# Optimization experiments

Hardware: AMD Instinct MI355X
Metric: run time of the kernel (lower is better)

Reference implementation:

```python
import jax, jax.numpy as jnp
import numpy as np

EP = 0.1
BETA = 10.0
ALPHA = 2.0
LMDA = 1.0
GROUP = 5  # 1 anchor + 4 positives per identity group


def setup_inputs() -> dict:
    key = jax.random.key(0)
    k1, k2 = jax.random.split(key)
    inputs = jax.random.normal(k1, (20480, 512), dtype=jnp.float32)
    targets = jax.random.randint(k2, (20480,), 0, 751, dtype=jnp.int64)
    return {"inputs": inputs, "targets": targets}


def reference(inputs, targets):
    B, D = inputs.shape
    N = B // GROUP  # number of anchor groups
    # f.data in torch detaches the anchor side; gradient flows only via inputs.T
    f = jax.lax.stop_gradient(inputs[0::GROUP])          # (N, D)
    sim = jnp.matmul(f, inputs.T)                         # (N, B)
    sim_r = sim.reshape(N, N, GROUP)                      # sim_r[k, j, r] = sim[k, 5j+r]

    idx = jnp.arange(N)
    # positives: sim[k, 5k+1 : 5k+5]  -> (N, 4)
    pos = sim_r[idx, idx, 1:GROUP]
    # own-group mask (anchor's entire group of 5 is excluded from negatives)
    own = (jnp.eye(N, dtype=bool))[:, :, None]            # (N, N, 1) broadcast over r

    neg_inf = jnp.finfo(sim.dtype).min
    neg_max = jnp.where(own, neg_inf, sim_r).max(axis=(1, 2))   # (N,)
    pos_min = pos.min(axis=1)                                    # (N,)

    # positive branch: keep pos_sim < neg_max + ep
    p_mask = pos < (neg_max[:, None] + EP)                       # (N, 4)
    loss_p = jnp.log1p(jnp.sum(jnp.where(p_mask, jnp.exp(-ALPHA * (pos - LMDA)), 0.0), axis=1)) / ALPHA

    # negative branch: keep neg_sim > pos_min - ep, over all other groups
    n_mask = (sim_r > (pos_min[:, None, None] - EP)) & (~own)    # (N, N, 5)
    loss_n = jnp.log1p(jnp.sum(jnp.where(n_mask, jnp.exp(BETA * (sim_r - LMDA)), 0.0), axis=(1, 2))) / BETA

    loss = jnp.sum(loss_p + loss_n) / N                          # matches loss / f.shape[0]
    p_num = jnp.sum(p_mask).astype(jnp.float32)
    n_num = jnp.sum(n_mask).astype(jnp.float32)
    p_ratio = p_num / (4.0 * N)
    n_ratio = n_num / (float(B - GROUP) * N)
    return loss, p_ratio, n_ratio
```

## Files before the change

### kernel.cpp

```cpp
#include <hip/hip_runtime.h>
#include <hip/hip_bf16.h>
#include <math.h>

#define NB    4096
#define BB    20480
#define DD    512
#define EPc    0.1f
#define BETAc  10.0f
#define ALPHAc 2.0f
#define LMDAc  1.0f
#define SHIFT  1400.0

typedef __attribute__((ext_vector_type(8))) short bf16x8;
typedef __attribute__((ext_vector_type(4))) float f32x4;
typedef unsigned int u32;

#define GLOAD16(gp, lp) \
    __builtin_amdgcn_global_load_lds((const __attribute__((address_space(1))) u32*)(gp), \
                                     (__attribute__((address_space(3))) u32*)(lp), 16, 0, 0)

__device__ __forceinline__ unsigned fenc(float x) {
    unsigned b = __float_as_uint(x);
    return (b & 0x80000000u) ? ~b : (b | 0x80000000u);
}
__device__ __forceinline__ float fdec(unsigned k) {
    unsigned b = (k & 0x80000000u) ? (k ^ 0x80000000u) : ~k;
    return __uint_as_float(b);
}

__device__ __forceinline__ void split2(float a, float b, u32* h, u32* l) {
    __hip_bfloat16 ha = __float2bfloat16(a);
    __hip_bfloat16 hb = __float2bfloat16(b);
    unsigned short ba, bb;
    __builtin_memcpy(&ba, &ha, 2); __builtin_memcpy(&bb, &hb, 2);
    float fa = __uint_as_float((u32)ba << 16);
    float fb = __uint_as_float((u32)bb << 16);
    __hip_bfloat16 la = __float2bfloat16(a - fa);
    __hip_bfloat16 lb = __float2bfloat16(b - fb);
    unsigned short ca, cb;
    __builtin_memcpy(&ca, &la, 2); __builtin_memcpy(&cb, &lb, 2);
    *h = (u32)ba | ((u32)bb << 16);
    *l = (u32)ca | ((u32)cb << 16);
}

__device__ __forceinline__ uint4 cvt8_sel(const float* __restrict__ src, bool lo_part) {
    float4 x0 = *(const float4*)(src);
    float4 x1 = *(const float4*)(src + 4);
    float xs[8] = {x0.x, x0.y, x0.z, x0.w, x1.x, x1.y, x1.z, x1.w};
    u32 w[4];
    #pragma unroll
    for (int p = 0; p < 4; ++p) {
        u32 h, l;
        split2(xs[2*p], xs[2*p+1], &h, &l);
        w[p] = lo_part ? l : h;
    }
    return make_uint4(w[0], w[1], w[2], w[3]);
}

__global__ __launch_bounds__(256) void packA_kernel(const float* __restrict__ inp,
        u32* __restrict__ apk)
{
    const u32 slot = blockIdx.x * 256 + threadIdx.x;
    const u32 lane = slot & 63;
    const u32 rest = slot >> 6;
    const u32 kc   = rest % 48;
    const u32 ablk = rest / 48;
    const int  i    = ablk * 16 + (lane & 15);
    const int  k0   = (kc % 16) * 32 + (lane >> 4) * 8;
    const bool lo_p = ((kc / 16) == 1);
    uint4 v = cvt8_sel(inp + (size_t)(5 * i) * DD + k0, lo_p);
    *(uint4*)(apk + (size_t)slot * 4) = v;
}

__global__ __launch_bounds__(256) void packB_kernel(const float* __restrict__ inp,
        u32* __restrict__ bpk)
{
    const u32 slot = blockIdx.x * 256 + threadIdx.x;
    const u32 lane = slot & 63;
    const u32 rest = slot >> 6;
    const u32 kc   = rest % 48;
    const u32 cblk = rest / 48;
    const int  r    = cblk * 16 + (lane & 15);
    const int  k0   = (kc % 16) * 32 + (lane >> 4) * 8;
    const bool lo_p = ((kc / 16) == 2);
    uint4 v = cvt8_sel(inp + (size_t)r * DD + k0, lo_p);
    *(uint4*)(bpk + (size_t)slot * 4) = v;
}

__global__ __launch_bounds__(256) void split_kernel(const float* __restrict__ inp,
        u32* __restrict__ hi, u32* __restrict__ lo)
{
    const size_t e = ((size_t)blockIdx.x * 256 + threadIdx.x) * 8;
    float4 x0 = *(const float4*)(inp + e);
    float4 x1 = *(const float4*)(inp + e + 4);
    u32 h[4], l[4];
    split2(x0.x, x0.y, &h[0], &l[0]);
    split2(x0.z, x0.w, &h[1], &l[1]);
    split2(x1.x, x1.y, &h[2], &l[2]);
    split2(x1.z, x1.w, &h[3], &l[3]);
    *(uint4*)(hi + e / 2) = make_uint4(h[0], h[1], h[2], h[3]);
    *(uint4*)(lo + e / 2) = make_uint4(l[0], l[1], l[2], l[3]);
}

__global__ __launch_bounds__(256) void pos_kernel(const float* __restrict__ inp,
        float* __restrict__ pos, float* __restrict__ posmin)
{
    const int wid  = threadIdx.x >> 6;
    const int lane = threadIdx.x & 63;
    const int i = blockIdx.x * 4 + wid;
    const float* f = inp + (size_t)(5 * i) * DD + lane * 8;
    float4 fa = *(const float4*)(f);
    float4 fb = *(const float4*)(f + 4);
    float pmin = INFINITY;
    #pragma unroll
    for (int g = 1; g < 5; ++g) {
        const float* x = inp + (size_t)(5 * i + g) * DD + lane * 8;
        float4 xa = *(const float4*)(x);
        float4 xb = *(const float4*)(x + 4);
        float s = fa.x*xa.x + fa.y*xa.y + fa.z*xa.z + fa.w*xa.w
                + fb.x*xb.x + fb.y*xb.y + fb.z*xb.z + fb.w*xb.w;
        #pragma unroll
        for (int m = 1; m < 64; m <<= 1) s += __shfl_xor(s, m, 64);
        if (lane == 0) pos[i * 4 + (g - 1)] = s;
        pmin = fminf(pmin, s);
    }
    if (lane == 0) posmin[i] = pmin;
}

__device__ __forceinline__ void row_epilogue(int i, int c0, int wc, int l15,
        float s0, float s1, float s2, float s3,
        const float* __restrict__ posmin, unsigned* __restrict__ negkey,
        double* __restrict__ msum, unsigned* __restrict__ cntn)
{
    const float th = posmin[i] - EPc;
    float vmax = -INFINITY;
    float lM   = -INFINITY;
    float lS   = 0.f;
    int   vcnt = 0;
    float sv[4] = {s0, s1, s2, s3};
    float args[4]; bool msk[4];
    #pragma unroll
    for (int fc = 0; fc < 4; ++fc) {
        const int c = c0 + wc + fc * 16 + l15;
        const float s = sv[fc];
        const bool nonown = ((c / 5) != i);
        msk[fc]  = nonown && (s > th);
        args[fc] = BETAc * (s - LMDAc);
        if (nonown)  vmax = fmaxf(vmax, s);
        if (msk[fc]) { vcnt += 1; lM = fmaxf(lM, args[fc]); }
    }
    #pragma unroll
    for (int fc = 0; fc < 4; ++fc)
        if (msk[fc]) lS += __expf(args[fc] - lM);
    #pragma unroll
    for (int m = 1; m < 16; m <<= 1) {
        vmax  = fmaxf(vmax, __shfl_xor(vmax, m, 64));
        vcnt += __shfl_xor(vcnt, m, 64);
        float oM = __shfl_xor(lM, m, 64);
        float oS = __shfl_xor(lS, m, 64);
        if (oS != 0.f) {
            if (lS == 0.f)      { lM = oM; lS = oS; }
            else if (lM >= oM)  { lS += oS * __expf(oM - lM); }
            else                { lS = oS + lS * __expf(lM - oM); lM = oM; }
        }
    }
    if (l15 == 0) {
        atomicMax(&negkey[i], fenc(vmax));
        atomicAdd(&cntn[i], (unsigned)vcnt);
        if (lS > 0.f) {
            double e = (double)lM - SHIFT;
            if (e > 690.0) e = 690.0;
            double Dv = exp(e) * (double)lS;
            if (!(Dv < 1e300)) Dv = 1e300;
            atomicAdd(&msum[i], Dv);
        }
    }
}

__global__ __launch_bounds__(256, 3) void sim_mfma10(const u32* __restrict__ apk,
        const u32* __restrict__ bpk, const float* __restrict__ posmin,
        unsigned* __restrict__ negkey, double* __restrict__ msum,
        unsigned* __restrict__ cntn)
{
    const int t    = threadIdx.x;
    const int lane = t & 63;
    const int w    = t >> 6;
    const int l15  = lane & 15;
    const int l4   = lane >> 4;

    const int bid   = blockIdx.x;
    const int xcd   = bid & 7;
    const int r_    = bid >> 3;
    const int chunk = r_ >> 4;
    const int pos   = r_ & 15;
    const int gc    = xcd * 40 + chunk;
    const int bi    = (gc & 7) * 4 + (pos & 3);
    const int bj    = (gc >> 3) * 4 + (pos >> 2);
    const int i0    = bi * 128;
    const int c0    = bj * 128;
    const int wr    = (w >> 1) * 64;
    const int wc    = (w & 1) * 64;

    const u32* pa[4];
    const u32* pb[4];
    #pragma unroll
    for (int f = 0; f < 4; ++f) {
        const int ablk = bi * 8 + (w >> 1) * 4 + f;
        const int cblk = bj * 8 + (w & 1) * 4 + f;
        pa[f] = apk + ((size_t)ablk * 48 * 64 + lane) * 4;
        pb[f] = bpk + ((size_t)cblk * 48 * 64 + lane) * 4;
    }

    f32x4 acc[4][4];
    #pragma unroll
    for (int a = 0; a < 4; ++a)
        #pragma unroll
        for (int b = 0; b < 4; ++b) acc[a][b] = (f32x4)0.f;

#define LOADF(AV, BV, KC) do {                                           \
    _Pragma("unroll")                                                    \
    for (int f_ = 0; f_ < 4; ++f_) (AV)[f_] = *(const bf16x8*)(pa[f_] + (KC) * 256); \
    _Pragma("unroll")                                                    \
    for (int f_ = 0; f_ < 4; ++f_) (BV)[f_] = *(const bf16x8*)(pb[f_] + (KC) * 256); \
} while (0)

#define MMB(AV, BV) do {                                                 \
    __builtin_amdgcn_s_setprio(1);                                       \
    _Pragma("unroll")                                                    \
    for (int fr_ = 0; fr_ < 4; ++fr_)                                    \
        _Pragma("unroll")                                                \
        for (int fc_ = 0; fc_ < 4; ++fc_)                                \
            acc[fr_][fc_] = __builtin_amdgcn_mfma_f32_16x16x32_bf16(     \
                (AV)[fr_], (BV)[fc_], acc[fr_][fc_], 0, 0, 0);           \
    __builtin_amdgcn_s_setprio(0);                                       \
} while (0)

    bf16x8 a0[4], b0[4], a1[4], b1[4];
    LOADF(a0, b0, 0);
    #pragma unroll 1
    for (int kc = 0; kc < 48; kc += 2) {
        LOADF(a1, b1, kc + 1);
        MMB(a0, b0);
        if (kc + 2 < 48) LOADF(a0, b0, kc + 2);
        MMB(a1, b1);
    }
#undef LOADF
#undef MMB

    #pragma unroll
    for (int fr = 0; fr < 4; ++fr) {
        #pragma unroll
        for (int reg = 0; reg < 4; ++reg) {
            const int i = i0 + wr + fr * 16 + l4 * 4 + reg;
            row_epilogue(i, c0, wc, l15,
                         acc[fr][0][reg], acc[fr][1][reg],
                         acc[fr][2][reg], acc[fr][3][reg],
                         posmin, negkey, msum, cntn);
        }
    }
}

__global__ __launch_bounds__(256) void sim_mfma7(const u32* __restrict__ hi,
        const u32* __restrict__ lo, const float* __restrict__ posmin,
        unsigned* __restrict__ negkey, double* __restrict__ msum,
        unsigned* __restrict__ cntn)
{
    __shared__ u32 As0[2048], Bs0[2048];
    __shared__ u32 As1[2048], Bs1[2048];

    const int t    = threadIdx.x;
    const int bj   = blockIdx.x % (BB / 128);
    const int bi   = blockIdx.x / (BB / 128);
    const int i0   = bi * 128;
    const int c0   = bj * 128;
    const int lane = t & 63;
    const int w    = t >> 6;
    const int wr   = (w >> 1) * 64;
    const int wc   = (w & 1) * 64;
    const int l15  = lane & 15;
    const int l4   = lane >> 4;

    const int srow = w * 32 + (lane >> 2);
    const int sc   = (lane & 3) ^ ((srow >> 1) & 3);
    const size_t rbA0 = (size_t)(5 * (i0 + srow))      * 1024 + sc * 16;
    const size_t rbA1 = (size_t)(5 * (i0 + srow + 16)) * 1024 + sc * 16;
    const size_t rbB0 = (size_t)(c0 + srow)      * 1024 + sc * 16;
    const size_t rbB1 = (size_t)(c0 + srow + 16) * 1024 + sc * 16;
    const int dL0 = (w * 32) * 16;
    const int dL1 = (w * 32 + 16) * 16;

#define STAGE(AS, BS, s) do {                                            \
    const int p_ = (s) >> 4;                                             \
    const size_t kk_ = (size_t)((s) & 15) * 64;                          \
    const char* bA_ = (const char*)(p_ == 1 ? lo : hi);                  \
    const char* bB_ = (const char*)(p_ == 2 ? lo : hi);                  \
    GLOAD16(bA_ + rbA0 + kk_, (AS) + dL0);                               \
    GLOAD16(bA_ + rbA1 + kk_, (AS) + dL1);                               \
    GLOAD16(bB_ + rbB0 + kk_, (BS) + dL0);                               \
    GLOAD16(bB_ + rbB1 + kk_, (BS) + dL1);                               \
} while (0)

    f32x4 acc[4][4];
    #pragma unroll
    for (int a = 0; a < 4; ++a)
        #pragma unroll
        for (int b = 0; b < 4; ++b) acc[a][b] = (f32x4)0.f;

    int aoff[4], boff[4];
    #pragma unroll
    for (int f = 0; f < 4; ++f) {
        const int row = wr + f * 16 + l15;
        const int col = wc + f * 16 + l15;
        aoff[f] = row * 64 + ((l4 ^ ((row >> 1) & 3)) * 16);
        boff[f] = col * 64 + ((l4 ^ ((col >> 1) & 3)) * 16);
    }

#define COMPUTE(AS, BS) do {                                             \
    bf16x8 bv[4];                                                        \
    _Pragma("unroll")                                                    \
    for (int fc = 0; fc < 4; ++fc)                                       \
        bv[fc] = *(const bf16x8*)((const char*)(BS) + boff[fc]);         \
    _Pragma("unroll")                                                    \
    for (int fr = 0; fr < 4; ++fr) {                                     \
        bf16x8 av = *(const bf16x8*)((const char*)(AS) + aoff[fr]);      \
        _Pragma("unroll")                                                \
        for (int fc = 0; fc < 4; ++fc)                                   \
            acc[fr][fc] = __builtin_amdgcn_mfma_f32_16x16x32_bf16(av, bv[fc], acc[fr][fc], 0, 0, 0); \
    }                                                                    \
} while (0)

#define VMCNT4  asm volatile("s_waitcnt vmcnt(4)" ::: "memory")
#define VMCNT0  asm volatile("s_waitcnt vmcnt(0)" ::: "memory")
#define MFENCE  asm volatile("" ::: "memory")
#define BARRIER __builtin_amdgcn_s_barrier()

    STAGE(As0, Bs0, 0);
    STAGE(As1, Bs1, 1);
    for (int it = 0; it < 23; ++it) {
        VMCNT4; BARRIER; MFENCE;
        COMPUTE(As0, Bs0);
        BARRIER; MFENCE;
        STAGE(As0, Bs0, 2 * it + 2);
        VMCNT4; BARRIER; MFENCE;
        COMPUTE(As1, Bs1);
        BARRIER; MFENCE;
        STAGE(As1, Bs1, 2 * it + 3);
    }
    VMCNT4; BARRIER; MFENCE;
    COMPUTE(As0, Bs0);
    VMCNT0; BARRIER; MFENCE;
    COMPUTE(As1, Bs1);

#undef STAGE
#undef COMPUTE
#undef VMCNT4
#undef VMCNT0
#undef MFENCE
#undef BARRIER

    #pragma unroll
    for (int fr = 0; fr < 4; ++fr) {
        #pragma unroll
        for (int reg = 0; reg < 4; ++reg) {
            const int i = i0 + wr + fr * 16 + l4 * 4 + reg;
            row_epilogue(i, c0, wc, l15,
                         acc[fr][0][reg], acc[fr][1][reg],
                         acc[fr][2][reg], acc[fr][3][reg],
                         posmin, negkey, msum, cntn);
        }
    }
}

__device__ __forceinline__ void cvt8(const float* __restrict__ src,
                                     uint4* __restrict__ dhi, uint4* __restrict__ dlo)
{
    float4 x0 = *(const float4*)(src);
    float4 x1 = *(const float4*)(src + 4);
    float xs[8] = {x0.x, x0.y, x0.z, x0.w, x1.x, x1.y, x1.z, x1.w};
    u32 h[4], l[4];
    #pragma unroll
    for (int p = 0; p < 4; ++p) split2(xs[2*p], xs[2*p+1], &h[p], &l[p]);
    *dhi = make_uint4(h[0], h[1], h[2], h[3]);
    *dlo = make_uint4(l[0], l[1], l[2], l[3]);
}

__global__ __launch_bounds__(256) void sim_mfma(const float* __restrict__ inp,
        const float* __restrict__ posmin, unsigned* __restrict__ negkey,
        double* __restrict__ msum, unsigned* __restrict__ cntn)
{
    __shared__ uint4 AsHi[128][4];
    __shared__ uint4 AsLo[128][4];
    __shared__ uint4 BsHi[128][4];
    __shared__ uint4 BsLo[128][4];

    const int t    = threadIdx.x;
    const int bj   = blockIdx.x % (BB / 128);
    const int bi   = blockIdx.x / (BB / 128);
    const int i0   = bi * 128;
    const int c0   = bj * 128;
    const int lane = t & 63;
    const int w    = t >> 6;
    const int wr   = (w >> 1) * 64;
    const int wc   = (w & 1) * 64;
    const int l15  = lane & 15;
    const int l4   = lane >> 4;

    f32x4 acc[4][4];
    #pragma unroll
    for (int a = 0; a < 4; ++a)
        #pragma unroll
        for (int b = 0; b < 4; ++b) acc[a][b] = (f32x4)0.f;

    const int r0  = t >> 2;
    const int ch0 = t & 3;

    for (int kb = 0; kb < DD; kb += 32) {
        __syncthreads();
        #pragma unroll
        for (int half = 0; half < 2; ++half) {
            const int row = r0 + half * 64;
            const int cs  = ch0 ^ ((row >> 2) & 3);
            cvt8(inp + (size_t)(5 * (i0 + row)) * DD + kb + ch0 * 8,
                 &AsHi[row][cs], &AsLo[row][cs]);
            cvt8(inp + (size_t)(c0 + row) * DD + kb + ch0 * 8,
                 &BsHi[row][cs], &BsLo[row][cs]);
        }
        __syncthreads();

        bf16x8 bh[4], bl[4];
        #pragma unroll
        for (int fc = 0; fc < 4; ++fc) {
            const int col = wc + fc * 16 + l15;
            const int cs  = l4 ^ ((col >> 2) & 3);
            bh[fc] = *(const bf16x8*)&BsHi[col][cs];
            bl[fc] = *(const bf16x8*)&BsLo[col][cs];
        }
        #pragma unroll
        for (int fr = 0; fr < 4; ++fr) {
            const int row = wr + fr * 16 + l15;
            const int cs  = l4 ^ ((row >> 2) & 3);
            bf16x8 ah = *(const bf16x8*)&AsHi[row][cs];
            bf16x8 al = *(const bf16x8*)&AsLo[row][cs];
            #pragma unroll
            for (int fc = 0; fc < 4; ++fc) {
                acc[fr][fc] = __builtin_amdgcn_mfma_f32_16x16x32_bf16(ah, bh[fc], acc[fr][fc], 0, 0, 0);
                acc[fr][fc] = __builtin_amdgcn_mfma_f32_16x16x32_bf16(ah, bl[fc], acc[fr][fc], 0, 0, 0);
                acc[fr][fc] = __builtin_amdgcn_mfma_f32_16x16x32_bf16(al, bh[fc], acc[fr][fc], 0, 0, 0);
            }
        }
    }

    #pragma unroll
    for (int fr = 0; fr < 4; ++fr) {
        #pragma unroll
        for (int reg = 0; reg < 4; ++reg) {
            const int i = i0 + wr + fr * 16 + l4 * 4 + reg;
            row_epilogue(i, c0, wc, l15,
                         acc[fr][0][reg], acc[fr][1][reg],
                         acc[fr][2][reg], acc[fr][3][reg],
                         posmin, negkey, msum, cntn);
        }
    }
}

__global__ __launch_bounds__(1024) void fin_kernel(const float* __restrict__ pos,
        const unsigned* __restrict__ negkey, const double* __restrict__ msum,
        const unsigned* __restrict__ cntn, float* __restrict__ out)
{
    const int t = threadIdx.x;
    double lossAcc = 0.0;
    int pAcc = 0, nAcc = 0;
    for (int r = t; r < NB; r += 1024) {
        const float negmax = fdec(negkey[r]);
        const float thr = negmax + EPc;
        float Mp = -INFINITY; int pc = 0;
        float pa[4]; bool pm[4];
        #pragma unroll
        for (int g = 0; g < 4; ++g) {
            const float p = pos[r * 4 + g];
            pa[g] = -ALPHAc * (p - LMDAc);
            pm[g] = (p < thr);
            if (pm[g]) { pc += 1; Mp = fmaxf(Mp, pa[g]); }
        }
        double lp = 0.0;
        if (pc > 0) {
            float sp = 0.f;
            #pragma unroll
            for (int g = 0; g < 4; ++g)
                if (pm[g]) sp += __expf(pa[g] - Mp);
            double a = (double)Mp + log((double)sp);
            lp = (a > 30.0 ? a : log1p(exp(a))) / (double)ALPHAc;
        }
        double ln = 0.0;
        double Dsum = msum[r];
        if (Dsum > 0.0) {
            double a = SHIFT + log(Dsum);
            ln = (a > 30.0 ? a : log1p(exp(a))) / (double)BETAc;
        }
        double contrib = lp + ln;
        if (!(contrib < 1e30)) contrib = 1e30;
        lossAcc += contrib;
        pAcc += pc;
        nAcc += (int)cntn[r];
    }
    __shared__ double sl[1024];
    __shared__ int    sp_[1024];
    __shared__ int    sn_[1024];
    sl[t] = lossAcc; sp_[t] = pAcc; sn_[t] = nAcc;
    __syncthreads();
    for (int s = 512; s > 0; s >>= 1) {
        if (t < s) { sl[t] += sl[t + s]; sp_[t] += sp_[t + s]; sn_[t] += sn_[t + s]; }
        __syncthreads();
    }
    if (t == 0) {
        double loss = sl[0] / 4096.0;
        if (!(loss < 1e30)) loss = 1e30;
        out[0] = (float)loss;
        out[1] = (float)sp_[0] / 16384.0f;
        out[2] = (float)sn_[0] / 83865600.0f;
    }
}

extern "C" void kernel_launch(void* const* d_in, const int* in_sizes, int n_in,
                              void* d_out, int out_size, void* d_ws, size_t ws_size,
                              hipStream_t stream)
{
    (void)in_sizes; (void)n_in; (void)out_size;
    const float* inp = (const float*)d_in[0];
    char* ws = (char*)d_ws;
    float*    pos    = (float*)   (ws);
    float*    posmin = (float*)   (ws + 65536);
    unsigned* negkey = (unsigned*)(ws + 81920);
    double*   msum   = (double*)  (ws + 98304);
    unsigned* cntn   = (unsigned*)(ws + 131072);
    float*    out    = (float*)d_out;

    u32* apk = (u32*)(ws + 147456);
    u32* bpk = (u32*)(ws + 147456 + (size_t)NB * 1536 * 2);
    u32* hi  = (u32*)(ws + 147456);
    u32* lo  = (u32*)(ws + 147456 + (size_t)BB * DD * 2);

    const size_t need_pack = 147456 + ((size_t)NB + BB) * 1536 * 2;
    const size_t need_mid  = 147456 + (size_t)BB * DD * 4;

    hipMemsetAsync(ws + 81920, 0, 65536, stream);
    hipLaunchKernelGGL(pos_kernel, dim3(NB / 4), dim3(256), 0, stream, inp, pos, posmin);

    if (ws_size >= need_pack) {
        hipLaunchKernelGGL(packA_kernel, dim3(NB / 16 * 48 * 64 / 256), dim3(256), 0, stream, inp, apk);
        hipLaunchKernelGGL(packB_kernel, dim3(BB / 16 * 48 * 64 / 256), dim3(256), 0, stream, inp, bpk);
        hipLaunchKernelGGL(sim_mfma10, dim3((NB / 128) * (BB / 128)), dim3(256), 0, stream,
                           apk, bpk, posmin, negkey, msum, cntn);
    } else if (ws_size >= need_mid) {
        hipLaunchKernelGGL(split_kernel, dim3(BB * DD / (256 * 8)), dim3(256), 0, stream,
                           inp, hi, lo);
        hipLaunchKernelGGL(sim_mfma7, dim3((NB / 128) * (BB / 128)), dim3(256), 0, stream,
                           hi, lo, posmin, negkey, msum, cntn);
    } else {
        hipLaunchKernelGGL(sim_mfma, dim3((NB / 128) * (BB / 128)), dim3(256), 0, stream,
                           inp, posmin, negkey, msum, cntn);
    }
    hipLaunchKernelGGL(fin_kernel, dim3(1), dim3(1024), 0, stream, pos, negkey, msum, cntn, out);
}
```

Baseline: 390.3 us.

## Triple-buffer packed operand loads with inline-asm global loads and explicit vmcnt waits

Replaces the double-buffered register prefetch in the packed MFMA kernel with a three-stage pipeline. Loads are issued through inline assembly with immediate offsets, and explicit s_waitcnt vmcnt counts plus sched barriers give finer control over when data must arrive. The goal is to keep more global loads in flight and hide memory latency behind the MFMA blocks. The extra register buffers push the launch-bounds occupancy hint from 3 to 2 blocks, trading occupancy for deeper per-wave pipelining. Manual waitcnt management is fragile if the compiler inserts other memory ops.

```diff
diff --git a/kernel.cpp b/kernel.cpp
--- a/kernel.cpp
+++ b/kernel.cpp
@@ -177,7 +177,7 @@
     }
 }
 
-__global__ __launch_bounds__(256, 3) void sim_mfma10(const u32* __restrict__ apk,
+__global__ __launch_bounds__(256, 2) void sim_mfma12(const u32* __restrict__ apk,
         const u32* __restrict__ bpk, const float* __restrict__ posmin,
         unsigned* __restrict__ negkey, double* __restrict__ msum,
         unsigned* __restrict__ cntn)
@@ -201,15 +201,16 @@
     const int wr    = (w >> 1) * 64;
     const int wc    = (w & 1) * 64;
 
-    const u32* pa[4];
-    const u32* pb[4];
-    #pragma unroll
-    for (int f = 0; f < 4; ++f) {
-        const int ablk = bi * 8 + (w >> 1) * 4 + f;
-        const int cblk = bj * 8 + (w & 1) * 4 + f;
-        pa[f] = apk + ((size_t)ablk * 48 * 64 + lane) * 4;
-        pb[f] = bpk + ((size_t)cblk * 48 * 64 + lane) * 4;
-    }
+    const int ab = bi * 8 + (w >> 1) * 4;
+    const int cb = bj * 8 + (w & 1) * 4;
+    const u32* pA0 = apk + ((size_t)(ab + 0) * 3072 + lane * 4) + 256;
+    const u32* pA1 = apk + ((size_t)(ab + 1) * 3072 + lane * 4) + 256;
+    const u32* pA2 = apk + ((size_t)(ab + 2) * 3072 + lane * 4) + 256;
+    const u32* pA3 = apk + ((size_t)(ab + 3) * 3072 + lane * 4) + 256;
+    const u32* pB0 = bpk + ((size_t)(cb + 0) * 3072 + lane * 4) + 256;
+    const u32* pB1 = bpk + ((size_t)(cb + 1) * 3072 + lane * 4) + 256;
+    const u32* pB2 = bpk + ((size_t)(cb + 2) * 3072 + lane * 4) + 256;
+    const u32* pB3 = bpk + ((size_t)(cb + 3) * 3072 + lane * 4) + 256;
 
     f32x4 acc[4][4];
     #pragma unroll
@@ -217,11 +218,22 @@
         #pragma unroll
         for (int b = 0; b < 4; ++b) acc[a][b] = (f32x4)0.f;
 
-#define LOADF(AV, BV, KC) do {                                           \
-    _Pragma("unroll")                                                    \
-    for (int f_ = 0; f_ < 4; ++f_) (AV)[f_] = *(const bf16x8*)(pa[f_] + (KC) * 256); \
-    _Pragma("unroll")                                                    \
-    for (int f_ = 0; f_ < 4; ++f_) (BV)[f_] = *(const bf16x8*)(pb[f_] + (KC) * 256); \
+    bf16x8 a0[4], b0[4], a1[4], b1[4], a2[4], b2[4];
+
+#define GLD(dst, ptr, OFFTOK) \
+    asm volatile("global_load_dwordx4 %0, %1, off offset:" OFFTOK \
+                 : "=&v"(dst) : "v"(ptr) : "memory")
+
+#define LOADSET(AV, BV, OFFTOK) do {                                     \
+    GLD((AV)[0], pA0, OFFTOK); GLD((AV)[1], pA1, OFFTOK);                \
+    GLD((AV)[2], pA2, OFFTOK); GLD((AV)[3], pA3, OFFTOK);                \
+    GLD((BV)[0], pB0, OFFTOK); GLD((BV)[1], pB1, OFFTOK);                \
+    GLD((BV)[2], pB2, OFFTOK); GLD((BV)[3], pB3, OFFTOK);                \
+} while (0)
+
+#define VMW(NTOK) do {                                                   \
+    asm volatile("s_waitcnt vmcnt(" NTOK ")" ::: "memory");              \
+    __builtin_amdgcn_sched_barrier(0);                                   \
 } while (0)
 
 #define MMB(AV, BV) do {                                                 \
@@ -235,16 +247,26 @@
     __builtin_amdgcn_s_setprio(0);                                       \
 } while (0)
 
-    bf16x8 a0[4], b0[4], a1[4], b1[4];
-    LOADF(a0, b0, 0);
+    LOADSET(a0, b0, "-1024");
+    LOADSET(a1, b1, "0");
     #pragma unroll 1
-    for (int kc = 0; kc < 48; kc += 2) {
-        LOADF(a1, b1, kc + 1);
-        MMB(a0, b0);
-        if (kc + 2 < 48) LOADF(a0, b0, kc + 2);
-        MMB(a1, b1);
-    }
-#undef LOADF
+    for (int it = 0; it < 15; ++it) {
+        LOADSET(a2, b2, "1024");
+        VMW("16"); MMB(a0, b0);
+        LOADSET(a0, b0, "2048");
+        VMW("16"); MMB(a1, b1);
+        LOADSET(a1, b1, "3072");
+        VMW("16"); MMB(a2, b2);
+        pA0 += 768; pA1 += 768; pA2 += 768; pA3 += 768;
+        pB0 += 768; pB1 += 768; pB2 += 768; pB3 += 768;
+    }
+    LOADSET(a2, b2, "1024");
+    VMW("16"); MMB(a0, b0);
+    VMW("8");  MMB(a1, b1);
+    VMW("0");  MMB(a2, b2);
+#undef GLD
+#undef LOADSET
+#undef VMW
 #undef MMB
 
     #pragma unroll
@@ -549,7 +571,7 @@
     if (ws_size >= need_pack) {
         hipLaunchKernelGGL(packA_kernel, dim3(NB / 16 * 48 * 64 / 256), dim3(256), 0, stream, inp, apk);
         hipLaunchKernelGGL(packB_kernel, dim3(BB / 16 * 48 * 64 / 256), dim3(256), 0, stream, inp, bpk);
-        hipLaunchKernelGGL(sim_mfma10, dim3((NB / 128) * (BB / 128)), dim3(256), 0, stream,
+        hipLaunchKernelGGL(sim_mfma12, dim3((NB / 128) * (BB / 128)), dim3(256), 0, stream,
                            apk, bpk, posmin, negkey, msum, cntn);
     } else if (ws_size >= need_mid) {
         hipLaunchKernelGGL(split_kernel, dim3(BB * DD / (256 * 8)), dim3(256), 0, stream,
```

Result: slower. 408.7 us (+4.7%).
